# Performance work log

Hardware: AMD Instinct MI355X
Metric: run time of the kernel (lower is better)

The kernel has to match this reference:

```python
import jax, jax.numpy as jnp
import numpy as np

B, S, G = 128, 128, 2000          # batch, set_size, n_genes
NH, H, NLAT = 256, 4, 64          # n_hidden, n_heads, n_latent
HD = NH // H                      # head_dim = 64
NGAT = 2                          # n_gat_layers
LN_EPS = 1e-5


def _layer_norm(x, g, b):
    mu = jnp.mean(x, axis=-1, keepdims=True)
    var = jnp.var(x, axis=-1, keepdims=True)
    return (x - mu) * jax.lax.rsqrt(var + LN_EPS) * g + b


def setup_inputs() -> dict:
    key = jax.random.key(0)
    ks = jax.random.split(key, 12)
    x_set = jax.random.normal(ks[0], (B, S, G), dtype=jnp.float32)
    adj = jax.random.randint(ks[1], (B, S, S), 0, 2).astype(jnp.int32)
    # guarantee self-loops so no softmax row is fully masked
    adj = jnp.maximum(adj, jnp.eye(S, dtype=jnp.int32)[None])
    w = 0.02
    return {
        "x_set": x_set,
        "adj": adj,
        "W_in": jax.random.normal(ks[2], (G, NH), dtype=jnp.float32) * w,
        "b_in": jnp.zeros((NH,), jnp.float32),
        "ln_in_g": jnp.ones((NH,), jnp.float32),
        "ln_in_b": jnp.zeros((NH,), jnp.float32),
        "Wg": jax.random.normal(ks[3], (NGAT, NH, NH), dtype=jnp.float32) * w,
        "a_src": jax.random.normal(ks[4], (NGAT, H, HD), dtype=jnp.float32) * 0.1,
        "a_dst": jax.random.normal(ks[5], (NGAT, H, HD), dtype=jnp.float32) * 0.1,
        "a_edge": jax.random.normal(ks[6], (NGAT, H, HD), dtype=jnp.float32) * 0.1,
        "We": jax.random.normal(ks[7], (NGAT, NH, NH), dtype=jnp.float32) * w,
        "ln_g": jnp.ones((NGAT, NH), jnp.float32),
        "ln_b": jnp.zeros((NGAT, NH), jnp.float32),
        "Wz": jax.random.normal(ks[8], (NH, NLAT), dtype=jnp.float32) * w,
        "bz": jnp.zeros((NLAT,), jnp.float32),
    }


def reference(x_set, adj, W_in, b_in, ln_in_g, ln_in_b, Wg, a_src, a_dst,
              a_edge, We, ln_g, ln_b, Wz, bz):
    # input_proj: Linear -> LayerNorm -> GELU (dropout = identity in eval)
    h = jax.nn.gelu(_layer_norm(x_set @ W_in + b_in, ln_in_g, ln_in_b),
                    approximate=False)
    masked = (adj == 0)[..., None]                       # (B,S,S,1)
    for l in range(NGAT):
        hp = (h @ Wg[l]).reshape(B, S, H, HD)            # W(x) per head
        s_src = jnp.einsum('bshd,hd->bsh', hp, a_src[l])
        s_dst = jnp.einsum('bshd,hd->bsh', hp, a_dst[l])
        # edge features e_ij = h_i - h_j; edge_proj is linear (no bias), so
        # <proj(h_i - h_j), a_edge> = es_i - es_j  (exactly the original math,
        # without materializing the (B,S,S,NH) tensor)
        es = jnp.einsum('bshd,hd->bsh', (h @ We[l]).reshape(B, S, H, HD),
                        a_edge[l])
        logits = (s_src + es)[:, :, None, :] + (s_dst - es)[:, None, :, :]
        logits = jnp.where(logits >= 0, logits, 0.2 * logits)  # LeakyReLU(0.2)
        logits = jnp.where(masked, -jnp.inf, logits)
        attn = jax.nn.softmax(logits, axis=2)            # over neighbors j
        out = jnp.einsum('bijh,bjhd->bihd', attn, hp).reshape(B, S, NH)
        h = jax.nn.gelu(_layer_norm(out, ln_g[l], ln_b[l]), approximate=False)
    z_all = h @ Wz + bz                                  # (B,S,NLAT)
    return z_all
```

## Files before the change

kernel.cpp:

```cpp
#include <hip/hip_runtime.h>
#include <hip/hip_bf16.h>
#include <cstdint>
#include <cstddef>

#define BB   128
#define SS   128
#define GG   2000
#define NHID 256
#define NHEAD 4
#define HDIM 64
#define NLAT 64
#define KPAD 2048

typedef __attribute__((ext_vector_type(4))) float f32x4;
typedef __attribute__((ext_vector_type(8))) short short8;
typedef __attribute__((ext_vector_type(4))) short bfs4;
typedef __attribute__((ext_vector_type(8))) __bf16 bf8_t;

static __device__ __forceinline__ bf8_t as_bf8(short8 s){
  union { short8 s; bf8_t b; } u; u.s = s; return u.b;
}

static __device__ __forceinline__ unsigned short f2bf(float f){
  union { float f; unsigned u; } x; x.f = f;
  unsigned r = x.u + 0x7fffu + ((x.u >> 16) & 1u);
  return (unsigned short)(r >> 16);
}

#define GLOAD_LDS16(g, l) __builtin_amdgcn_global_load_lds( \
    (const __attribute__((address_space(1))) unsigned int*)(g), \
    (__attribute__((address_space(3))) unsigned int*)(l), 16, 0, 0)

__global__ __launch_bounds__(256) void k_x2bf(
    const float* __restrict__ X, unsigned short* __restrict__ Xb)
{
  const int gid = blockIdx.x * 256 + threadIdx.x;
  const int row = gid >> 8;
  const int c8  = gid & 255;
  const int k0  = c8 << 3;
  short8 v;
  if (k0 < GG) {
    f32x4 a0 = *(const f32x4*)(X + (size_t)row * GG + k0);
    f32x4 a1 = *(const f32x4*)(X + (size_t)row * GG + k0 + 4);
    v[0]=(short)f2bf(a0.x); v[1]=(short)f2bf(a0.y); v[2]=(short)f2bf(a0.z); v[3]=(short)f2bf(a0.w);
    v[4]=(short)f2bf(a1.x); v[5]=(short)f2bf(a1.y); v[6]=(short)f2bf(a1.z); v[7]=(short)f2bf(a1.w);
  } else {
#pragma unroll
    for (int t = 0; t < 8; ++t) v[t] = 0;
  }
  *(short8*)(Xb + (size_t)row * KPAD + k0) = v;
}

__global__ __launch_bounds__(256) void k_transconv(
    const float* __restrict__ W, unsigned short* __restrict__ Wt,
    int K, int N, int Kpad)
{
  int idx = blockIdx.x * 256 + threadIdx.x;
  if (idx >= N * Kpad) return;
  int n = idx / Kpad, k = idx - n * Kpad;
  float v = (k < K) ? W[(size_t)k * N + n] : 0.f;
  Wt[idx] = f2bf(v);
}

__global__ __launch_bounds__(256) void k_adjpack(
    const int* __restrict__ adj, unsigned long long* __restrict__ abits)
{
  const int wid  = blockIdx.x * 4 + (threadIdx.x >> 6);
  const int lane = threadIdx.x & 63;
  int v = adj[(size_t)wid * 64 + lane];
  unsigned long long m = __ballot(v != 0);
  if (lane == 0) abits[wid] = m;
}

__global__ __launch_bounds__(512, 1) void k_gemm_in(
    const unsigned short* __restrict__ A,
    const unsigned short* __restrict__ Bt,
    float* __restrict__ Out)
{
  __shared__ __align__(16) unsigned short Ab[2][8][64][8];
  __shared__ __align__(16) unsigned short Bb[2][16][64][8];
  const int tid = threadIdx.x, l = tid & 63, w = tid >> 6;
  const int wr = w >> 2, wc = w & 3;
  const int m0 = blockIdx.x * 128;
  const int kbase0 = blockIdx.y * 1024;
  const int nsteps = 32;

  const unsigned short* aB = A  + (size_t)(m0 + (l & 15)) * KPAD + kbase0 + (l >> 4) * 8;
  const unsigned short* bB = Bt + (size_t)(l & 15) * KPAD + kbase0 + (l >> 4) * 8;

  f32x4 acc[4][4];
#pragma unroll
  for (int i = 0; i < 4; ++i)
#pragma unroll
    for (int j = 0; j < 4; ++j) acc[i][j] = (f32x4)(0.f);

  auto stage = [&](int buf, int koff) {
#pragma unroll
    for (int q = 0; q < 3; ++q) {
      const int tile = w * 3 + q;
      if (tile < 8) {
        GLOAD_LDS16(aB + (size_t)(16 * tile) * KPAD + koff, &Ab[buf][tile][0][0]);
      } else {
        GLOAD_LDS16(bB + (size_t)(16 * (tile - 8)) * KPAD + koff, &Bb[buf][tile - 8][0][0]);
      }
    }
  };

  stage(0, 0);
  __syncthreads();

  for (int s = 0; s < nsteps; ++s) {
    const int cur = s & 1;
    if (s + 1 < nsteps) stage(cur ^ 1, (s + 1) * 32);
    short8 af[4], bfv[4];
#pragma unroll
    for (int i = 0; i < 4; ++i) af[i]  = *(const short8*)&Ab[cur][4 * wr + i][l][0];
#pragma unroll
    for (int j = 0; j < 4; ++j) bfv[j] = *(const short8*)&Bb[cur][4 * wc + j][l][0];
#pragma unroll
    for (int i = 0; i < 4; ++i)
#pragma unroll
      for (int j = 0; j < 4; ++j)
        acc[i][j] = __builtin_amdgcn_mfma_f32_16x16x32_bf16(
            as_bf8(af[i]), as_bf8(bfv[j]), acc[i][j], 0, 0, 0);
    __syncthreads();
  }

  float* outp = Out + (size_t)blockIdx.y * ((size_t)BB * SS * NHID);
  const int orow = m0 + (wr << 6) + ((l >> 4) << 2);
  const int ocol = (wc << 6) + (l & 15);
#pragma unroll
  for (int i = 0; i < 4; ++i)
#pragma unroll
    for (int j = 0; j < 4; ++j) {
      const int row = orow + i * 16, col = ocol + j * 16;
#pragma unroll
      for (int r = 0; r < 4; ++r)
        outp[(size_t)(row + r) * NHID + col] = acc[i][j][r];
    }
}

__global__ __launch_bounds__(256, 2) void k_gemm_hp(
    const unsigned short* __restrict__ A,
    const unsigned short* __restrict__ Bt,
    unsigned short* __restrict__ hpT)
{
  __shared__ __align__(16) unsigned short Ab[2][8][64][8];
  __shared__ __align__(16) unsigned short Bb[2][8][64][8];
  const int tid = threadIdx.x, l = tid & 63, w = tid >> 6;
  const int wr = w >> 1, wc = w & 1;
  const int m0 = blockIdx.x * 128, n0 = blockIdx.y * 128;

  const int rA = l & 15;
  const unsigned short* aB = A  + (size_t)(m0 + rA) * NHID + (l >> 4) * 8;
  const unsigned short* bB = Bt + (size_t)(n0 + rA) * NHID + (l >> 4) * 8;

  f32x4 acc[4][4];
#pragma unroll
  for (int i = 0; i < 4; ++i)
#pragma unroll
    for (int j = 0; j < 4; ++j) acc[i][j] = (f32x4)(0.f);

  auto stage = [&](int buf, int koff) {
#pragma unroll
    for (int t = 0; t < 2; ++t) {
      const int ia = 2 * w + t;
      GLOAD_LDS16(aB + (size_t)(16 * ia) * NHID + koff, &Ab[buf][ia][0][0]);
      GLOAD_LDS16(bB + (size_t)(16 * ia) * NHID + koff, &Bb[buf][ia][0][0]);
    }
  };

  stage(0, 0);
  __syncthreads();

  for (int s = 0; s < 8; ++s) {
    const int cur = s & 1;
    if (s + 1 < 8) stage(cur ^ 1, (s + 1) * 32);
    short8 af[4], bfv[4];
#pragma unroll
    for (int i = 0; i < 4; ++i) af[i]  = *(const short8*)&Ab[cur][4 * wr + i][l][0];
#pragma unroll
    for (int j = 0; j < 4; ++j) bfv[j] = *(const short8*)&Bb[cur][4 * wc + j][l][0];
#pragma unroll
    for (int i = 0; i < 4; ++i)
#pragma unroll
      for (int j = 0; j < 4; ++j)
        acc[i][j] = __builtin_amdgcn_mfma_f32_16x16x32_bf16(
            as_bf8(af[i]), as_bf8(bfv[j]), acc[i][j], 0, 0, 0);
    __syncthreads();
  }

  const int bidx = m0 >> 7;
  const int i0 = (wr << 6) + ((l >> 4) << 2);
  const int ocol = n0 + (wc << 6) + (l & 15);
  unsigned short* hb = hpT + (size_t)bidx * NHID * SS;
#pragma unroll
  for (int i = 0; i < 4; ++i)
#pragma unroll
    for (int j = 0; j < 4; ++j) {
      const int col = ocol + j * 16;
      bfs4 o;
#pragma unroll
      for (int r = 0; r < 4; ++r) o[r] = (short)f2bf(acc[i][j][r]);
      *(bfs4*)&hb[(size_t)col * SS + i0 + i * 16] = o;
    }
}

__global__ __launch_bounds__(256) void k_ln_fuse(
    const float* __restrict__ X0, const float* __restrict__ X1,
    const float* __restrict__ bias, const float* __restrict__ g,
    const float* __restrict__ b, unsigned short* __restrict__ out_bf,
    float* __restrict__ out_f32, const float* __restrict__ u,
    float* __restrict__ c1, float* __restrict__ c2)
{
  const int tid = threadIdx.x, l = tid & 63, w = tid >> 6;
  const f32x4 gg = *(const f32x4*)(g + l * 4);
  const f32x4 bb = *(const f32x4*)(b + l * 4);
  f32x4 bias4 = (f32x4)(0.f);
  if (bias) bias4 = *(const f32x4*)(bias + l * 4);
  f32x4 u1v[4], u2v[4];
  if (u) {
#pragma unroll
    for (int t = 0; t < 4; ++t) {
      u1v[t] = *(const f32x4*)(u + (size_t)(4 * l + t) * 4);
      u2v[t] = *(const f32x4*)(u + 1024 + (size_t)(4 * l + t) * 4);
    }
  }
  for (int it = 0; it < 4; ++it) {
    const int row = blockIdx.x * 16 + w * 4 + it;
    f32x4 x = *(const f32x4*)(X0 + (size_t)row * NHID + l * 4);
    if (X1) {
      f32x4 x1 = *(const f32x4*)(X1 + (size_t)row * NHID + l * 4);
      x.x += x1.x; x.y += x1.y; x.z += x1.z; x.w += x1.w;
    }
    x.x += bias4.x; x.y += bias4.y; x.z += bias4.z; x.w += bias4.w;
    float s  = x.x + x.y + x.z + x.w;
    float sq = x.x * x.x + x.y * x.y + x.z * x.z + x.w * x.w;
#pragma unroll
    for (int m = 1; m < 64; m <<= 1) { s += __shfl_xor(s, m); sq += __shfl_xor(sq, m); }
    const float mu   = s * (1.f / 256.f);
    const float var  = sq * (1.f / 256.f) - mu * mu;
    const float rstd = rsqrtf(var + 1e-5f);
    float y[4];
#pragma unroll
    for (int t = 0; t < 4; ++t) {
      float yy = (x[t] - mu) * rstd * gg[t] + bb[t];
      y[t] = 0.5f * yy * (1.f + erff(yy * 0.70710678118654752f));
    }
    if (out_bf) {
      bfs4 o;
#pragma unroll
      for (int t = 0; t < 4; ++t) o[t] = (short)f2bf(y[t]);
      *(bfs4*)(out_bf + (size_t)row * NHID + l * 4) = o;
    }
    if (out_f32) {
      f32x4 o; o.x = y[0]; o.y = y[1]; o.z = y[2]; o.w = y[3];
      *(f32x4*)(out_f32 + (size_t)row * NHID + l * 4) = o;
    }
    if (u) {
      float d1[4] = {0.f,0.f,0.f,0.f}, d2[4] = {0.f,0.f,0.f,0.f};
#pragma unroll
      for (int t = 0; t < 4; ++t)
#pragma unroll
        for (int h = 0; h < 4; ++h) {
          d1[h] += y[t] * u1v[t][h];
          d2[h] += y[t] * u2v[t][h];
        }
#pragma unroll
      for (int h = 0; h < 4; ++h) {
#pragma unroll
        for (int m = 1; m < 64; m <<= 1) {
          d1[h] += __shfl_xor(d1[h], m);
          d2[h] += __shfl_xor(d2[h], m);
        }
      }
      if (l == 0) {
#pragma unroll
        for (int h = 0; h < 4; ++h) {
          c1[(size_t)row * 4 + h] = d1[h];
          c2[(size_t)row * 4 + h] = d2[h];
        }
      }
    }
  }
}

__global__ __launch_bounds__(256, 1) void k_proj(
    const float* __restrict__ Wg, const float* __restrict__ We,
    const float* __restrict__ asrc, const float* __restrict__ adst,
    const float* __restrict__ aedge, float* __restrict__ u)
{
  const int lyr = blockIdx.x;
  const int k = threadIdx.x;
  const float* Wgl = Wg + (size_t)lyr * NHID * NHID;
  const float* Wel = We + (size_t)lyr * NHID * NHID;
  float* u1 = u + (size_t)lyr * 2048;
  float* u2 = u1 + 1024;
#pragma unroll
  for (int h = 0; h < 4; ++h) {
    float ss = 0.f, sd = 0.f, se = 0.f;
    const float* wg  = Wgl + k * NHID + h * 64;
    const float* we  = Wel + k * NHID + h * 64;
    const float* pas = asrc + lyr * NHEAD * HDIM + h * 64;
    const float* pad_ = adst + lyr * NHEAD * HDIM + h * 64;
    const float* pae = aedge + lyr * NHEAD * HDIM + h * 64;
#pragma unroll 4
    for (int d = 0; d < 64; ++d) {
      ss += wg[d] * pas[d];
      sd += wg[d] * pad_[d];
      se += we[d] * pae[d];
    }
    u1[k * 4 + h] = ss + se;
    u2[k * 4 + h] = sd - se;
  }
}

__global__ __launch_bounds__(256) void k_attn2(
    const unsigned short* __restrict__ hpT, const float* __restrict__ c1,
    const float* __restrict__ c2, const unsigned long long* __restrict__ abits,
    float* __restrict__ out)
{
  __shared__ __align__(16) unsigned short Pb[4][8][64][8];
  __shared__ __align__(16) unsigned short Vb[4][4][64][8];
  __shared__ float s1[128], s2[128];
  __shared__ float mbuf[2][128], sbuf[2][128], invsum[128];
  const int head = blockIdx.x, b = blockIdx.y;
  const int tid = threadIdx.x, w = tid >> 6, l = tid & 63;

  if (tid < 128) {
    const int m = b * SS + tid;
    s1[tid] = c1[m * 4 + head];
    s2[tid] = c2[m * 4 + head];
  }
  {
    const unsigned short* hb = hpT + ((size_t)b * NHID + head * 64) * SS;
#pragma unroll
    for (int q = 0; q < 4; ++q) {
      const int tile = w * 4 + q;
      const int kstep = tile >> 2, nt = tile & 3;
      const unsigned short* src =
          hb + (size_t)(nt * 16 + (l & 15)) * SS + kstep * 32 + (l >> 4) * 8;
      GLOAD_LDS16(src, &Vb[kstep][nt][0][0]);
    }
  }
  __syncthreads();

  const int i = tid & 127, half = tid >> 7;
  const float s1v = s1[i];
  const unsigned long long bits = abits[((size_t)b * SS + i) * 2 + half];

  float ma[4] = {-3.0e38f, -3.0e38f, -3.0e38f, -3.0e38f};
#pragma unroll
  for (int jl = 0; jl < 64; ++jl) {
    float x  = s1v + s2[half * 64 + jl];
    float lk = fmaxf(x, 0.2f * x);
    float xm = ((bits >> jl) & 1ull) ? lk : -3.0e38f;
    ma[jl & 3] = fmaxf(ma[jl & 3], xm);
  }
  mbuf[half][i] = fmaxf(fmaxf(ma[0], ma[1]), fmaxf(ma[2], ma[3]));
  __syncthreads();
  const float mrow = fmaxf(mbuf[0][i], mbuf[1][i]);

  float sa[4] = {0.f, 0.f, 0.f, 0.f};
#pragma unroll
  for (int grp = 0; grp < 8; ++grp) {
    short8 pv;
#pragma unroll
    for (int e = 0; e < 8; ++e) {
      const int jl = grp * 8 + e;
      float x  = s1v + s2[half * 64 + jl];
      float lk = fmaxf(x, 0.2f * x);
      float xm = ((bits >> jl) & 1ull) ? lk : -3.0e38f;
      float p  = exp2f((xm - mrow) * 1.4426950408889634f);
      sa[e & 3] += p;
      pv[e] = (short)f2bf(p);
    }
    const int j = half * 64 + grp * 8;
    const int kstep = j >> 5, g = (j >> 3) & 3;
    *(short8*)&Pb[kstep][i >> 4][(g << 4) | (i & 15)][0] = pv;
  }
  sbuf[half][i] = (sa[0] + sa[1]) + (sa[2] + sa[3]);
  __syncthreads();
  if (tid < 128) invsum[tid] = 1.f / (sbuf[0][tid] + sbuf[1][tid]);
  __syncthreads();

  f32x4 acc[2][4];
#pragma unroll
  for (int ii = 0; ii < 2; ++ii)
#pragma unroll
    for (int nt = 0; nt < 4; ++nt) acc[ii][nt] = (f32x4)(0.f);
#pragma unroll
  for (int kstep = 0; kstep < 4; ++kstep) {
    short8 bv[4];
#pragma unroll
    for (int nt = 0; nt < 4; ++nt) bv[nt] = *(const short8*)&Vb[kstep][nt][l][0];
#pragma unroll
    for (int ii = 0; ii < 2; ++ii) {
      short8 af = *(const short8*)&Pb[kstep][2 * w + ii][l][0];
#pragma unroll
      for (int nt = 0; nt < 4; ++nt)
        acc[ii][nt] = __builtin_amdgcn_mfma_f32_16x16x32_bf16(
            as_bf8(af), as_bf8(bv[nt]), acc[ii][nt], 0, 0, 0);
    }
  }

  float* ob = out + (size_t)(b * SS) * NHID + head * 64;
#pragma unroll
  for (int ii = 0; ii < 2; ++ii) {
    const int it = 2 * w + ii;
#pragma unroll
    for (int r = 0; r < 4; ++r) {
      const int row = it * 16 + (l >> 4) * 4 + r;
      const float inv = invsum[row];
#pragma unroll
      for (int nt = 0; nt < 4; ++nt)
        ob[(size_t)row * NHID + nt * 16 + (l & 15)] = acc[ii][nt][r] * inv;
    }
  }
}

__global__ __launch_bounds__(256, 1) void k_zgemm(
    const float* __restrict__ hmat, const float* __restrict__ Wz,
    const float* __restrict__ bz, float* __restrict__ Z)
{
  __shared__ __align__(16) float hrows[64 * 256];
  const int tid = threadIdx.x, w = tid >> 6, l = tid & 63;
  const int r0 = blockIdx.x * 64;
  const f32x4* src = (const f32x4*)(hmat + (size_t)r0 * NHID);
#pragma unroll
  for (int rep = 0; rep < 16; ++rep)
    ((f32x4*)hrows)[rep * 256 + tid] = src[rep * 256 + tid];
  __syncthreads();
  const float bzv = bz[l];
  const int rbase = w * 16;
#pragma unroll
  for (int pass = 0; pass < 4; ++pass) {
    float acc0 = 0.f, acc1 = 0.f, acc2 = 0.f, acc3 = 0.f;
    const float* h0 = &hrows[(rbase + pass * 4) * 256];
#pragma unroll 8
    for (int k = 0; k < 256; ++k) {
      float wv = Wz[k * 64 + l];
      acc0 += h0[k] * wv;
      acc1 += h0[256 + k] * wv;
      acc2 += h0[512 + k] * wv;
      acc3 += h0[768 + k] * wv;
    }
    float* zp = Z + (size_t)(r0 + rbase + pass * 4) * 64 + l;
    zp[0]   = acc0 + bzv;
    zp[64]  = acc1 + bzv;
    zp[128] = acc2 + bzv;
    zp[192] = acc3 + bzv;
  }
}

extern "C" void kernel_launch(void* const* d_in, const int* in_sizes, int n_in,
                              void* d_out, int out_size, void* d_ws, size_t ws_size,
                              hipStream_t stream)
{
  const float* x_set   = (const float*)d_in[0];
  const int*   adj     = (const int*)d_in[1];
  const float* W_in    = (const float*)d_in[2];
  const float* b_in    = (const float*)d_in[3];
  const float* ln_in_g = (const float*)d_in[4];
  const float* ln_in_b = (const float*)d_in[5];
  const float* Wg      = (const float*)d_in[6];
  const float* a_src   = (const float*)d_in[7];
  const float* a_dst   = (const float*)d_in[8];
  const float* a_edge  = (const float*)d_in[9];
  const float* We      = (const float*)d_in[10];
  const float* ln_g    = (const float*)d_in[11];
  const float* ln_b    = (const float*)d_in[12];
  const float* Wz      = (const float*)d_in[13];
  const float* bz      = (const float*)d_in[14];
  float* zout = (float*)d_out;

  const int M = BB * SS;

  char* base = (char*)d_ws;
  size_t off = 0;
  auto alloc = [&](size_t bytes) { char* p = base + off; off += (bytes + 255) & ~(size_t)255; return p; };
  unsigned short* Xb    = (unsigned short*)alloc((size_t)M * KPAD * 2);
  float*          P     = (float*)alloc((size_t)M * NHID * 4 * 2);
  unsigned short* hbf   = (unsigned short*)alloc((size_t)M * NHID * 2);
  unsigned short* wt_in = (unsigned short*)alloc((size_t)NHID * KPAD * 2);
  unsigned short* wgt   = (unsigned short*)alloc((size_t)NHID * NHID * 2);
  float*          u     = (float*)alloc(2 * 2048 * 4);
  float*          c1    = (float*)alloc((size_t)M * 4 * 4);
  float*          c2    = (float*)alloc((size_t)M * 4 * 4);
  unsigned long long* abits = (unsigned long long*)alloc((size_t)BB * SS * 2 * 8);
  unsigned short* hpT = Xb;
  float* bufA = (float*)Xb + (size_t)M * NHID;
  float* hfin = P;

  k_x2bf<<<dim3((M * (KPAD / 8)) / 256), dim3(256), 0, stream>>>(x_set, Xb);
  k_transconv<<<dim3((NHID * KPAD) / 256), dim3(256), 0, stream>>>(
      W_in, wt_in, GG, NHID, KPAD);
  k_proj<<<dim3(2), dim3(256), 0, stream>>>(Wg, We, a_src, a_dst, a_edge, u);
  k_adjpack<<<dim3(BB * SS * 2 / 4), dim3(256), 0, stream>>>(adj, abits);
  k_gemm_in<<<dim3(M / 128, 2), dim3(512), 0, stream>>>(Xb, wt_in, P);
  k_ln_fuse<<<dim3(M / 16), dim3(256), 0, stream>>>(
      P, P + (size_t)M * NHID, b_in, ln_in_g, ln_in_b, hbf, nullptr,
      u, c1, c2);

  for (int l = 0; l < 2; ++l) {
    const float* Wgl = Wg + (size_t)l * NHID * NHID;
    k_transconv<<<dim3((NHID * NHID) / 256), dim3(256), 0, stream>>>(
        Wgl, wgt, NHID, NHID, NHID);
    k_gemm_hp<<<dim3(M / 128, 2), dim3(256), 0, stream>>>(hbf, wgt, hpT);
    k_attn2<<<dim3(NHEAD, BB), dim3(256), 0, stream>>>(
        hpT, c1, c2, abits, bufA);
    if (l == 0) {
      k_ln_fuse<<<dim3(M / 16), dim3(256), 0, stream>>>(
          bufA, nullptr, nullptr, ln_g, ln_b, hbf, nullptr,
          u + 2048, c1, c2);
    } else {
      k_ln_fuse<<<dim3(M / 16), dim3(256), 0, stream>>>(
          bufA, nullptr, nullptr, ln_g + NHID, ln_b + NHID, nullptr, hfin,
          nullptr, nullptr, nullptr);
    }
  }

  k_zgemm<<<dim3(M / 64), dim3(256), 0, stream>>>(hfin, Wz, bz, zout);
}
```

Baseline: 230.5 us.

## Fuse fp32-to-bf16 input conversion into input GEMM and shrink GEMM tiles

Removes the separate k_x2bf pass that wrote a padded bf16 copy of x_set. The input GEMM now reads fp32 rows directly, converts them to bf16 in registers, and writes them into LDS, with a register-staged double buffer and the K split at 1000. This saves a full extra read and write of the large input. The M tile drops to 64 rows with 256 threads for both the input and hp GEMMs to raise the block count. In exchange, the A operand no longer uses async global-to-LDS loads, and each block gets less operand reuse.

```diff
diff --git a/kernel.cpp b/kernel.cpp
--- a/kernel.cpp
+++ b/kernel.cpp
@@ -11,6 +11,7 @@
 #define HDIM 64
 #define NLAT 64
 #define KPAD 2048
+#define KSPLIT 1000
 
 typedef __attribute__((ext_vector_type(4))) float f32x4;
 typedef __attribute__((ext_vector_type(8))) short short8;
@@ -30,26 +31,6 @@
 #define GLOAD_LDS16(g, l) __builtin_amdgcn_global_load_lds( \
     (const __attribute__((address_space(1))) unsigned int*)(g), \
     (__attribute__((address_space(3))) unsigned int*)(l), 16, 0, 0)
-
-__global__ __launch_bounds__(256) void k_x2bf(
-    const float* __restrict__ X, unsigned short* __restrict__ Xb)
-{
-  const int gid = blockIdx.x * 256 + threadIdx.x;
-  const int row = gid >> 8;
-  const int c8  = gid & 255;
-  const int k0  = c8 << 3;
-  short8 v;
-  if (k0 < GG) {
-    f32x4 a0 = *(const f32x4*)(X + (size_t)row * GG + k0);
-    f32x4 a1 = *(const f32x4*)(X + (size_t)row * GG + k0 + 4);
-    v[0]=(short)f2bf(a0.x); v[1]=(short)f2bf(a0.y); v[2]=(short)f2bf(a0.z); v[3]=(short)f2bf(a0.w);
-    v[4]=(short)f2bf(a1.x); v[5]=(short)f2bf(a1.y); v[6]=(short)f2bf(a1.z); v[7]=(short)f2bf(a1.w);
-  } else {
-#pragma unroll
-    for (int t = 0; t < 8; ++t) v[t] = 0;
-  }
-  *(short8*)(Xb + (size_t)row * KPAD + k0) = v;
-}
 
 __global__ __launch_bounds__(256) void k_transconv(
     const float* __restrict__ W, unsigned short* __restrict__ Wt,
@@ -72,21 +53,21 @@
   if (lane == 0) abits[wid] = m;
 }
 
-__global__ __launch_bounds__(512, 1) void k_gemm_in(
-    const unsigned short* __restrict__ A,
+__global__ __launch_bounds__(256, 2) void k_gemm_in(
+    const float* __restrict__ X,
     const unsigned short* __restrict__ Bt,
     float* __restrict__ Out)
 {
-  __shared__ __align__(16) unsigned short Ab[2][8][64][8];
+  __shared__ __align__(16) unsigned short Ab[2][4][64][8];
   __shared__ __align__(16) unsigned short Bb[2][16][64][8];
   const int tid = threadIdx.x, l = tid & 63, w = tid >> 6;
-  const int wr = w >> 2, wc = w & 3;
-  const int m0 = blockIdx.x * 128;
-  const int kbase0 = blockIdx.y * 1024;
+  const int m0 = blockIdx.x * 64;
+  const int kbase = blockIdx.y * KSPLIT;
   const int nsteps = 32;
 
-  const unsigned short* aB = A  + (size_t)(m0 + (l & 15)) * KPAD + kbase0 + (l >> 4) * 8;
-  const unsigned short* bB = Bt + (size_t)(l & 15) * KPAD + kbase0 + (l >> 4) * 8;
+  const int akg8 = (l >> 4) * 8;
+  const float* aP = X + (size_t)(m0 + (l & 15) + 16 * w) * GG + kbase + akg8;
+  const unsigned short* bB = Bt + (size_t)(l & 15) * KPAD + kbase + akg8;
 
   f32x4 acc[4][4];
 #pragma unroll
@@ -94,41 +75,62 @@
 #pragma unroll
     for (int j = 0; j < 4; ++j) acc[i][j] = (f32x4)(0.f);
 
-  auto stage = [&](int buf, int koff) {
-#pragma unroll
-    for (int q = 0; q < 3; ++q) {
-      const int tile = w * 3 + q;
-      if (tile < 8) {
-        GLOAD_LDS16(aB + (size_t)(16 * tile) * KPAD + koff, &Ab[buf][tile][0][0]);
-      } else {
-        GLOAD_LDS16(bB + (size_t)(16 * (tile - 8)) * KPAD + koff, &Bb[buf][tile - 8][0][0]);
-      }
+  auto stage_b = [&](int buf, int koff) {
+#pragma unroll
+    for (int q = 0; q < 4; ++q) {
+      const int tile = w * 4 + q;
+      GLOAD_LDS16(bB + (size_t)(16 * tile) * KPAD + koff, &Bb[buf][tile][0][0]);
     }
   };
-
-  stage(0, 0);
+  auto load_a = [&](int koff, f32x4& a0, f32x4& a1) {
+    if (koff + akg8 < KSPLIT) {
+      a0 = *(const f32x4*)(aP + koff);
+      a1 = *(const f32x4*)(aP + koff + 4);
+    } else {
+      a0 = (f32x4)(0.f); a1 = (f32x4)(0.f);
+    }
+  };
+  auto write_a = [&](int buf, const f32x4& a0, const f32x4& a1) {
+    short8 v;
+    v[0]=(short)f2bf(a0.x); v[1]=(short)f2bf(a0.y); v[2]=(short)f2bf(a0.z); v[3]=(short)f2bf(a0.w);
+    v[4]=(short)f2bf(a1.x); v[5]=(short)f2bf(a1.y); v[6]=(short)f2bf(a1.z); v[7]=(short)f2bf(a1.w);
+    *(short8*)&Ab[buf][w][l][0] = v;
+  };
+
+  {
+    f32x4 a0, a1;
+    stage_b(0, 0);
+    load_a(0, a0, a1);
+    write_a(0, a0, a1);
+  }
   __syncthreads();
 
   for (int s = 0; s < nsteps; ++s) {
     const int cur = s & 1;
-    if (s + 1 < nsteps) stage(cur ^ 1, (s + 1) * 32);
+    f32x4 a0, a1;
+    const bool more = (s + 1 < nsteps);
+    if (more) {
+      stage_b(cur ^ 1, (s + 1) * 32);
+      load_a((s + 1) * 32, a0, a1);
+    }
     short8 af[4], bfv[4];
 #pragma unroll
-    for (int i = 0; i < 4; ++i) af[i]  = *(const short8*)&Ab[cur][4 * wr + i][l][0];
-#pragma unroll
-    for (int j = 0; j < 4; ++j) bfv[j] = *(const short8*)&Bb[cur][4 * wc + j][l][0];
+    for (int i = 0; i < 4; ++i) af[i]  = *(const short8*)&Ab[cur][i][l][0];
+#pragma unroll
+    for (int j = 0; j < 4; ++j) bfv[j] = *(const short8*)&Bb[cur][4 * w + j][l][0];
 #pragma unroll
     for (int i = 0; i < 4; ++i)
 #pragma unroll
       for (int j = 0; j < 4; ++j)
         acc[i][j] = __builtin_amdgcn_mfma_f32_16x16x32_bf16(
             as_bf8(af[i]), as_bf8(bfv[j]), acc[i][j], 0, 0, 0);
+    if (more) write_a(cur ^ 1, a0, a1);
     __syncthreads();
   }
 
   float* outp = Out + (size_t)blockIdx.y * ((size_t)BB * SS * NHID);
-  const int orow = m0 + (wr << 6) + ((l >> 4) << 2);
-  const int ocol = (wc << 6) + (l & 15);
+  const int orow = m0 + ((l >> 4) << 2);
+  const int ocol = (w << 6) + (l & 15);
 #pragma unroll
   for (int i = 0; i < 4; ++i)
 #pragma unroll
@@ -145,28 +147,29 @@
     const unsigned short* __restrict__ Bt,
     unsigned short* __restrict__ hpT)
 {
-  __shared__ __align__(16) unsigned short Ab[2][8][64][8];
+  __shared__ __align__(16) unsigned short Ab[2][4][64][8];
   __shared__ __align__(16) unsigned short Bb[2][8][64][8];
   const int tid = threadIdx.x, l = tid & 63, w = tid >> 6;
-  const int wr = w >> 1, wc = w & 1;
-  const int m0 = blockIdx.x * 128, n0 = blockIdx.y * 128;
-
-  const int rA = l & 15;
-  const unsigned short* aB = A  + (size_t)(m0 + rA) * NHID + (l >> 4) * 8;
-  const unsigned short* bB = Bt + (size_t)(n0 + rA) * NHID + (l >> 4) * 8;
-
-  f32x4 acc[4][4];
+  const int m0 = blockIdx.x * 64, n0 = blockIdx.y * 128;
+
+  const unsigned short* aB = A  + (size_t)(m0 + (l & 15)) * NHID + (l >> 4) * 8;
+  const unsigned short* bB = Bt + (size_t)(n0 + (l & 15)) * NHID + (l >> 4) * 8;
+
+  f32x4 acc[4][2];
 #pragma unroll
   for (int i = 0; i < 4; ++i)
 #pragma unroll
-    for (int j = 0; j < 4; ++j) acc[i][j] = (f32x4)(0.f);
+    for (int j = 0; j < 2; ++j) acc[i][j] = (f32x4)(0.f);
 
   auto stage = [&](int buf, int koff) {
 #pragma unroll
-    for (int t = 0; t < 2; ++t) {
-      const int ia = 2 * w + t;
-      GLOAD_LDS16(aB + (size_t)(16 * ia) * NHID + koff, &Ab[buf][ia][0][0]);
-      GLOAD_LDS16(bB + (size_t)(16 * ia) * NHID + koff, &Bb[buf][ia][0][0]);
+    for (int q = 0; q < 3; ++q) {
+      const int t = w * 3 + q;
+      if (t < 4) {
+        GLOAD_LDS16(aB + (size_t)(16 * t) * NHID + koff, &Ab[buf][t][0][0]);
+      } else {
+        GLOAD_LDS16(bB + (size_t)(16 * (t - 4)) * NHID + koff, &Bb[buf][t - 4][0][0]);
+      }
     }
   };
 
@@ -176,33 +179,32 @@
   for (int s = 0; s < 8; ++s) {
     const int cur = s & 1;
     if (s + 1 < 8) stage(cur ^ 1, (s + 1) * 32);
-    short8 af[4], bfv[4];
-#pragma unroll
-    for (int i = 0; i < 4; ++i) af[i]  = *(const short8*)&Ab[cur][4 * wr + i][l][0];
-#pragma unroll
-    for (int j = 0; j < 4; ++j) bfv[j] = *(const short8*)&Bb[cur][4 * wc + j][l][0];
+    short8 af[4], bfv[2];
+#pragma unroll
+    for (int i = 0; i < 4; ++i) af[i]  = *(const short8*)&Ab[cur][i][l][0];
+#pragma unroll
+    for (int j = 0; j < 2; ++j) bfv[j] = *(const short8*)&Bb[cur][2 * w + j][l][0];
 #pragma unroll
     for (int i = 0; i < 4; ++i)
 #pragma unroll
-      for (int j = 0; j < 4; ++j)
+      for (int j = 0; j < 2; ++j)
         acc[i][j] = __builtin_amdgcn_mfma_f32_16x16x32_bf16(
             as_bf8(af[i]), as_bf8(bfv[j]), acc[i][j], 0, 0, 0);
     __syncthreads();
   }
 
   const int bidx = m0 >> 7;
-  const int i0 = (wr << 6) + ((l >> 4) << 2);
-  const int ocol = n0 + (wc << 6) + (l & 15);
+  const int rb0  = (m0 & 127) + ((l >> 4) << 2);
   unsigned short* hb = hpT + (size_t)bidx * NHID * SS;
 #pragma unroll
   for (int i = 0; i < 4; ++i)
 #pragma unroll
-    for (int j = 0; j < 4; ++j) {
-      const int col = ocol + j * 16;
+    for (int j = 0; j < 2; ++j) {
+      const int col = n0 + (2 * w + j) * 16 + (l & 15);
       bfs4 o;
 #pragma unroll
       for (int r = 0; r < 4; ++r) o[r] = (short)f2bf(acc[i][j][r]);
-      *(bfs4*)&hb[(size_t)col * SS + i0 + i * 16] = o;
+      *(bfs4*)&hb[(size_t)col * SS + rb0 + i * 16] = o;
     }
 }
 
@@ -479,25 +481,23 @@
   char* base = (char*)d_ws;
   size_t off = 0;
   auto alloc = [&](size_t bytes) { char* p = base + off; off += (bytes + 255) & ~(size_t)255; return p; };
-  unsigned short* Xb    = (unsigned short*)alloc((size_t)M * KPAD * 2);
   float*          P     = (float*)alloc((size_t)M * NHID * 4 * 2);
   unsigned short* hbf   = (unsigned short*)alloc((size_t)M * NHID * 2);
+  unsigned short* hpT   = (unsigned short*)alloc((size_t)M * NHID * 2);
+  float*          bufA  = (float*)alloc((size_t)M * NHID * 4);
   unsigned short* wt_in = (unsigned short*)alloc((size_t)NHID * KPAD * 2);
   unsigned short* wgt   = (unsigned short*)alloc((size_t)NHID * NHID * 2);
   float*          u     = (float*)alloc(2 * 2048 * 4);
   float*          c1    = (float*)alloc((size_t)M * 4 * 4);
   float*          c2    = (float*)alloc((size_t)M * 4 * 4);
   unsigned long long* abits = (unsigned long long*)alloc((size_t)BB * SS * 2 * 8);
-  unsigned short* hpT = Xb;
-  float* bufA = (float*)Xb + (size_t)M * NHID;
   float* hfin = P;
 
-  k_x2bf<<<dim3((M * (KPAD / 8)) / 256), dim3(256), 0, stream>>>(x_set, Xb);
   k_transconv<<<dim3((NHID * KPAD) / 256), dim3(256), 0, stream>>>(
       W_in, wt_in, GG, NHID, KPAD);
   k_proj<<<dim3(2), dim3(256), 0, stream>>>(Wg, We, a_src, a_dst, a_edge, u);
   k_adjpack<<<dim3(BB * SS * 2 / 4), dim3(256), 0, stream>>>(adj, abits);
-  k_gemm_in<<<dim3(M / 128, 2), dim3(512), 0, stream>>>(Xb, wt_in, P);
+  k_gemm_in<<<dim3(M / 64, 2), dim3(256), 0, stream>>>(x_set, wt_in, P);
   k_ln_fuse<<<dim3(M / 16), dim3(256), 0, stream>>>(
       P, P + (size_t)M * NHID, b_in, ln_in_g, ln_in_b, hbf, nullptr,
       u, c1, c2);
@@ -506,7 +506,7 @@
     const float* Wgl = Wg + (size_t)l * NHID * NHID;
     k_transconv<<<dim3((NHID * NHID) / 256), dim3(256), 0, stream>>>(
         Wgl, wgt, NHID, NHID, NHID);
-    k_gemm_hp<<<dim3(M / 128, 2), dim3(256), 0, stream>>>(hbf, wgt, hpT);
+    k_gemm_hp<<<dim3(M / 64, 2), dim3(256), 0, stream>>>(hbf, wgt, hpT);
     k_attn2<<<dim3(NHEAD, BB), dim3(256), 0, stream>>>(
         hpT, c1, c2, abits, bufA);
     if (l == 0) {
```

New measurement: 202.2 us. -12.3%, faster.
